# Kernel optimization log

Hardware: AMD Instinct MI355X
Metric: run time of the kernel (lower is better)

## Reference

```python
import jax, jax.numpy as jnp
import numpy as np
import math

B, T, C, D = 8, 2048, 1024, 1024
N_LAYER, LAYER_ID = 24, 12


def setup_inputs() -> dict:
    key = jax.random.key(0)
    ks = jax.random.split(key, 5)
    r01 = LAYER_ID / (N_LAYER - 1)
    r10 = 1.0 - LAYER_ID / N_LAYER
    ddd = np.arange(C, dtype=np.float64) / C                      # (C,)
    h = np.arange(D, dtype=np.float64)
    decay_speed = -5 + 8 * (h / (D - 1)) ** (0.7 + 1.3 * r01)     # time_decay init
    zigzag = ((np.arange(D) + 1) % 3 - 1) * 0.5
    time_first = np.log(0.3) + zigzag
    scale = C ** -0.5
    return {
        "x": jax.random.normal(ks[0], (B, T, C), jnp.float32),
        "time_decay": jnp.asarray(decay_speed, jnp.float32),
        "time_first": jnp.asarray(time_first, jnp.float32),
        "time_mix_k": jnp.asarray(ddd ** r10, jnp.float32),
        "time_mix_v": jnp.asarray(ddd ** r10 + 0.3 * r01, jnp.float32),
        "time_mix_r": jnp.asarray(ddd ** (0.5 * r10), jnp.float32),
        "Wk": jax.random.normal(ks[1], (D, C), jnp.float32) * scale,
        "Wv": jax.random.normal(ks[2], (D, C), jnp.float32) * scale,
        "Wr": jax.random.normal(ks[3], (D, C), jnp.float32) * scale,
        "Wo": jax.random.normal(ks[4], (C, D), jnp.float32) * scale,
    }


def _wkv(time_decay, time_first, k, v):
    # wkv_t = (e^{u+k_t} v_t + A_{t-1}) / (e^{u+k_t} + B_{t-1})
    # A_t = e^w A_{t-1} + e^{k_t} v_t ;  B_t likewise with v=1 ;  w = -exp(time_decay)
    # Exactly the math of the original conv1d-with-exp-curve trick, in O(T).
    ew = jnp.exp(-jnp.exp(time_decay))   # (D,)
    eu = jnp.exp(time_first)             # (D,)
    ek = jnp.exp(k)                      # [B,T,D]
    ekv = ek * v

    def step(carry, inp):
        a, b = carry                     # [B,D] each
        ekt, ekvt = inp                  # [B,D] each
        out = (eu * ekvt + a) / (eu * ekt + b)
        return (ew * a + ekvt, ew * b + ekt), out

    init = (jnp.zeros_like(ek[:, 0]), jnp.zeros_like(ek[:, 0]))
    xs = (jnp.swapaxes(ek, 0, 1), jnp.swapaxes(ekv, 0, 1))  # [T,B,D]
    _, out = jax.lax.scan(step, init, xs)
    return jnp.swapaxes(out, 0, 1)       # [B,T,D]


def reference(x, time_decay, time_first, time_mix_k, time_mix_v, time_mix_r, Wk, Wv, Wr, Wo):
    # time_shift: prepend zero row, drop last (ZeroPad2d((0,0,1,-1)))
    xx = jnp.pad(x, ((0, 0), (1, 0), (0, 0)))[:, :-1]
    xk = x * time_mix_k + xx * (1 - time_mix_k)
    xv = x * time_mix_v + xx * (1 - time_mix_v)
    xr = x * time_mix_r + xx * (1 - time_mix_r)
    k = jnp.einsum('btc,dc->btd', xk, Wk)
    v = jnp.einsum('btc,dc->btd', xv, Wv)
    sr = jax.nn.sigmoid(jnp.einsum('btc,dc->btd', xr, Wr))
    rwkv = sr * _wkv(time_decay, time_first, k, v)
    return jnp.einsum('btd,cd->btc', rwkv, Wo)
```

## Files before the change

kernel.cpp:

```cpp
#include <hip/hip_runtime.h>
#include <cstdint>
#include <cstddef>

#define Bb 8
#define Tt 2048
#define Cc 1024
#define Dd 1024
#define Mm (Bb*Tt)
#define CL 64
#define NCH (Tt/CL)


typedef __bf16  bf16x8  __attribute__((ext_vector_type(8)));
typedef float   floatx4 __attribute__((ext_vector_type(4)));

__device__ __forceinline__ ushort f2bf(float f) {
    unsigned u = __float_as_uint(f);
    u = (u + 0x7FFF + ((u >> 16) & 1)) >> 16;
    return (ushort)u;
}
__device__ __forceinline__ float bf2f(ushort u) {
    return __uint_as_float(((unsigned)u) << 16);
}

__device__ __forceinline__ void load_lds16(const void* g, void* l) {
    __builtin_amdgcn_global_load_lds((__attribute__((address_space(1))) void*)(g),
                                     (__attribute__((address_space(3))) void*)(l),
                                     16, 0, 0);
}

__global__ __launch_bounds__(256) void prep_mix3(
        const float* __restrict__ x,
        const float* __restrict__ mk, const float* __restrict__ mv,
        const float* __restrict__ mr,
        ushort* __restrict__ xk, ushort* __restrict__ xv, ushort* __restrict__ xr) {
    int i  = blockIdx.x * 256 + threadIdx.x;
    int cq = i & (Cc / 8 - 1);
    int m  = i >> 7;
    int t  = m & (Tt - 1);
    float xc[8], xp[8];
    *(float4*)&xc[0] = ((const float4*)x)[i * 2];
    *(float4*)&xc[4] = ((const float4*)x)[i * 2 + 1];
    if (t != 0) {
        *(float4*)&xp[0] = ((const float4*)x)[(i - Cc / 8) * 2];
        *(float4*)&xp[4] = ((const float4*)x)[(i - Cc / 8) * 2 + 1];
    } else {
#pragma unroll
        for (int j = 0; j < 8; j++) xp[j] = 0.f;
    }
    float wk[8], wv[8], wr[8];
    *(float4*)&wk[0] = ((const float4*)mk)[cq * 2];
    *(float4*)&wk[4] = ((const float4*)mk)[cq * 2 + 1];
    *(float4*)&wv[0] = ((const float4*)mv)[cq * 2];
    *(float4*)&wv[4] = ((const float4*)mv)[cq * 2 + 1];
    *(float4*)&wr[0] = ((const float4*)mr)[cq * 2];
    *(float4*)&wr[4] = ((const float4*)mr)[cq * 2 + 1];
    ushort ok[8], ov[8], orr[8];
#pragma unroll
    for (int j = 0; j < 8; j++) {
        float d = xc[j] - xp[j];
        ok[j]  = f2bf(xp[j] + d * wk[j]);
        ov[j]  = f2bf(xp[j] + d * wv[j]);
        orr[j] = f2bf(xp[j] + d * wr[j]);
    }
    ((ulonglong2*)xk)[i] = *(const ulonglong2*)ok;
    ((ulonglong2*)xv)[i] = *(const ulonglong2*)ov;
    ((ulonglong2*)xr)[i] = *(const ulonglong2*)orr;
}

__global__ __launch_bounds__(256) void cvt_w(
        const float* __restrict__ wk, const float* __restrict__ wv,
        const float* __restrict__ wr, const float* __restrict__ wo,
        ushort* __restrict__ ok, ushort* __restrict__ ov,
        ushort* __restrict__ orr, ushort* __restrict__ oo) {
    int i = blockIdx.x * 256 + threadIdx.x;
    int sel = i >> 18;
    int j = i & ((1 << 18) - 1);
    const float* s = sel == 0 ? wk : sel == 1 ? wv : sel == 2 ? wr : wo;
    ushort* d      = sel == 0 ? ok : sel == 1 ? ov : sel == 2 ? orr : oo;
    float4 f = ((const float4*)s)[j];
    ushort4 o;
    o.x = f2bf(f.x); o.y = f2bf(f.y); o.z = f2bf(f.z); o.w = f2bf(f.w);
    ((ushort4*)d)[j] = o;
}

struct GemmCore {
    floatx4 acc[4][4];
    int quad, fr, wave, wm, wn;

    __device__ __forceinline__ void run(
            const ushort* __restrict__ A, const ushort* __restrict__ Bw,
            long tm, long tn, int Kdim,
            __bf16* As, __bf16* Bs) {
        const int tid  = threadIdx.x;
        const int lane = tid & 63;
        quad = lane >> 4;
        fr   = lane & 15;
        wave = tid >> 6;
        wm   = (wave >> 1) * 64;
        wn   = (wave & 1) * 64;

        const int srow  = tid >> 2;
        const int spart = (tid & 3) ^ ((tid >> 3) & 3);
        const ushort* Ag0 = A + (tm + srow) * (long)Kdim + spart * 8;
        const ushort* Ag1 = Ag0 + 64 * (long)Kdim;
        const ushort* Bg0 = Bw + (tn + srow) * (long)Kdim + spart * 8;
        const ushort* Bg1 = Bg0 + 64 * (long)Kdim;
        const int swz = (fr >> 1) & 3;

        floatx4 zero = {0.f, 0.f, 0.f, 0.f};
#pragma unroll
        for (int a1 = 0; a1 < 4; a1++)
#pragma unroll
            for (int b1 = 0; b1 < 4; b1++) acc[a1][b1] = zero;

        const int niter = Kdim >> 5;
        load_lds16(Ag0, &As[wave * 512]);
        load_lds16(Ag1, &As[2048 + wave * 512]);
        load_lds16(Bg0, &Bs[wave * 512]);
        load_lds16(Bg1, &Bs[2048 + wave * 512]);

        for (int it = 0; it < niter; ++it) {
            const int cur = it & 1;
            __bf16* Ac = As + cur * 4096;
            __bf16* Bc = Bs + cur * 4096;
            __syncthreads();
            if (it + 1 < niter) {
                const int kt = (it + 1) << 5;
                __bf16* An = As + (cur ^ 1) * 4096;
                __bf16* Bn = Bs + (cur ^ 1) * 4096;
                load_lds16(Ag0 + kt, &An[wave * 512]);
                load_lds16(Ag1 + kt, &An[2048 + wave * 512]);
                load_lds16(Bg0 + kt, &Bn[wave * 512]);
                load_lds16(Bg1 + kt, &Bn[2048 + wave * 512]);
            }
            bf16x8 af[4], bfg[4];
#pragma unroll
            for (int mi = 0; mi < 4; mi++)
                af[mi] = *(const bf16x8*)&Ac[(wm + mi * 16 + fr) * 32 + (quad ^ swz) * 8];
#pragma unroll
            for (int ni = 0; ni < 4; ni++)
                bfg[ni] = *(const bf16x8*)&Bc[(wn + ni * 16 + fr) * 32 + (quad ^ swz) * 8];
#pragma unroll
            for (int mi = 0; mi < 4; mi++)
#pragma unroll
                for (int ni = 0; ni < 4; ni++)
                    acc[mi][ni] = __builtin_amdgcn_mfma_f32_16x16x32_bf16(
                        af[mi], bfg[ni], acc[mi][ni], 0, 0, 0);
        }
    }
};

template<int MODE>
__global__ __launch_bounds__(256) void gemm_nt(
        const ushort* __restrict__ A, const ushort* __restrict__ Bw,
        void* __restrict__ Co, int Ndim, int Kdim) {
    __shared__ __attribute__((aligned(16))) __bf16 As[2 * 128 * 32];
    __shared__ __attribute__((aligned(16))) __bf16 Bs[2 * 128 * 32];
    const long tm = (long)blockIdx.x * 128;
    const long tn = (long)blockIdx.y * 128;
    GemmCore g;
    g.run(A, Bw, tm, tn, Kdim, As, Bs);
#pragma unroll
    for (int mi = 0; mi < 4; mi++)
#pragma unroll
        for (int ni = 0; ni < 4; ni++)
#pragma unroll
            for (int r = 0; r < 4; r++) {
                long grow = tm + g.wm + mi * 16 + g.quad * 4 + r;
                long gcol = tn + g.wn + ni * 16 + g.fr;
                float v = g.acc[mi][ni][r];
                if (MODE == 2) v = 1.f / (1.f + __expf(-v));
                if (MODE == 0)      ((float*)Co)[grow * Ndim + gcol] = v;
                else if (MODE == 3) ((_Float16*)Co)[grow * Ndim + gcol] = (_Float16)v;
                else                ((ushort*)Co)[grow * Ndim + gcol] = f2bf(v);
            }
}

__global__ __launch_bounds__(256) void gemm3_nt(
        const ushort* __restrict__ xk, const ushort* __restrict__ xv,
        const ushort* __restrict__ xr,
        const ushort* __restrict__ wk, const ushort* __restrict__ wv,
        const ushort* __restrict__ wr,
        _Float16* __restrict__ kb, ushort* __restrict__ vb,
        ushort* __restrict__ sb) {
    __shared__ __attribute__((aligned(16))) __bf16 As[2 * 128 * 32];
    __shared__ __attribute__((aligned(16))) __bf16 Bs[2 * 128 * 32];
    const int proj = blockIdx.y >> 3;
    const long tm = (long)blockIdx.x * 128;
    const long tn = (long)(blockIdx.y & 7) * 128;
    const ushort* A  = proj == 0 ? xk : proj == 1 ? xv : xr;
    const ushort* Bw = proj == 0 ? wk : proj == 1 ? wv : wr;
    GemmCore g;
    g.run(A, Bw, tm, tn, Cc, As, Bs);
#pragma unroll
    for (int mi = 0; mi < 4; mi++)
#pragma unroll
        for (int ni = 0; ni < 4; ni++)
#pragma unroll
            for (int r = 0; r < 4; r++) {
                long grow = tm + g.wm + mi * 16 + g.quad * 4 + r;
                long gcol = tn + g.wn + ni * 16 + g.fr;
                long off = grow * Dd + gcol;
                float v = g.acc[mi][ni][r];
                if (proj == 0)      kb[off] = (_Float16)v;
                else if (proj == 1) vb[off] = f2bf(v);
                else                sb[off] = f2bf(1.f / (1.f + __expf(-v)));
            }
}

__global__ __launch_bounds__(256) void wkv_part(
        const _Float16* __restrict__ kb, const ushort* __restrict__ vb,
        const float* __restrict__ decay,
        float* __restrict__ pa, float* __restrict__ pb) {
    int gid = blockIdx.x * 256 + threadIdx.x;
    int d = gid & (Dd - 1);
    int c = (gid >> 10) & (NCH - 1);
    int b = gid >> 15;
    float ew = __expf(-__expf(decay[d]));
    size_t base = ((size_t)b * Tt + (size_t)c * CL) * Dd + d;
    float a = 0.f, bs = 0.f;
    for (int i0 = 0; i0 < CL; i0 += 8) {
        float kr[8], vr[8];
#pragma unroll
        for (int j = 0; j < 8; j++) {
            size_t idx = base + (size_t)(i0 + j) * Dd;
            kr[j] = (float)kb[idx]; vr[j] = bf2f(vb[idx]);
        }
#pragma unroll
        for (int j = 0; j < 8; j++) {
            float ek = __expf(kr[j]);
            a  = ew * a  + ek * vr[j];
            bs = ew * bs + ek;
        }
    }
    int sidx = c * (Bb * Dd) + b * Dd + d;
    pa[sidx] = a; pb[sidx] = bs;
}

__global__ __launch_bounds__(256) void wkv_prefix(
        const float* __restrict__ pa, const float* __restrict__ pb,
        const float* __restrict__ decay,
        float* __restrict__ sa, float* __restrict__ sb) {
    int gid = blockIdx.x * 256 + threadIdx.x;
    int d = gid & (Dd - 1);
    float ewL = __expf(-__expf(decay[d]) * (float)CL);
    float ca = 0.f, cb = 0.f;
#pragma unroll
    for (int c = 0; c < NCH; c++) {
        int idx = c * (Bb * Dd) + gid;
        sa[idx] = ca; sb[idx] = cb;
        ca = ewL * ca + pa[idx];
        cb = ewL * cb + pb[idx];
    }
}

__global__ __launch_bounds__(256) void wkv_chunk(
        const _Float16* __restrict__ kb, const ushort* __restrict__ vb,
        const ushort* __restrict__ sr,
        const float* __restrict__ decay, const float* __restrict__ tf,
        const float* __restrict__ sa, const float* __restrict__ sb,
        ushort* __restrict__ rw) {
    int gid = blockIdx.x * 256 + threadIdx.x;
    int d = gid & (Dd - 1);
    int c = (gid >> 10) & (NCH - 1);
    int b = gid >> 15;
    float ew = __expf(-__expf(decay[d]));
    float eu = __expf(tf[d]);
    int sidx = c * (Bb * Dd) + b * Dd + d;
    float a = sa[sidx], bs = sb[sidx];
    size_t base = ((size_t)b * Tt + (size_t)c * CL) * Dd + d;
    for (int i0 = 0; i0 < CL; i0 += 8) {
        float kr[8], vr[8], rr[8];
#pragma unroll
        for (int j = 0; j < 8; j++) {
            size_t idx = base + (size_t)(i0 + j) * Dd;
            kr[j] = (float)kb[idx]; vr[j] = bf2f(vb[idx]); rr[j] = bf2f(sr[idx]);
        }
#pragma unroll
        for (int j = 0; j < 8; j++) {
            float ek  = __expf(kr[j]);
            float ekv = ek * vr[j];
            float out = (eu * ekv + a) / (eu * ek + bs);
            a  = ew * a  + ekv;
            bs = ew * bs + ek;
            rw[base + (size_t)(i0 + j) * Dd] = f2bf(rr[j] * out);
        }
    }
}

extern "C" void kernel_launch(void* const* d_in, const int* in_sizes, int n_in,
                              void* d_out, int out_size, void* d_ws, size_t ws_size,
                              hipStream_t stream) {
    (void)in_sizes; (void)n_in; (void)out_size;
    const float* x  = (const float*)d_in[0];
    const float* td = (const float*)d_in[1];
    const float* tf = (const float*)d_in[2];
    const float* mk = (const float*)d_in[3];
    const float* mv = (const float*)d_in[4];
    const float* mr = (const float*)d_in[5];
    const float* Wk = (const float*)d_in[6];
    const float* Wv = (const float*)d_in[7];
    const float* Wr = (const float*)d_in[8];
    const float* Wo = (const float*)d_in[9];
    float* out = (float*)d_out;

    const size_t xsz = (size_t)Mm * Cc * 2;
    const size_t wsz = (size_t)Dd * Cc * 2;
    const size_t ssz = (size_t)Bb * NCH * Dd * 4;
    const size_t need_merged = 6 * xsz + 4 * wsz + 4 * ssz;

    char* p = (char*)d_ws;
    auto take = [&](size_t n) { char* r = p; p += n; return r; };
    ushort*   xk = (ushort*)take(xsz);
    ushort*   xv = (ushort*)take(xsz);
    ushort*   xr = (ushort*)take(xsz);
    _Float16* kb = (_Float16*)take(xsz);
    const bool merged = ws_size >= need_merged;
    ushort *vb, *sb, *rw;
    if (merged) {
        vb = (ushort*)take(xsz);
        sb = (ushort*)take(xsz);
        rw = xk;
    } else {
        vb = xk;
        sb = xv;
        rw = xr;
    }
    ushort* wk = (ushort*)take(wsz);
    ushort* wv = (ushort*)take(wsz);
    ushort* wr = (ushort*)take(wsz);
    ushort* wo = (ushort*)take(wsz);
    float*  pa = (float*)take(ssz);
    float*  pb = (float*)take(ssz);
    float*  sa = (float*)take(ssz);
    float*  sbst = (float*)take(ssz);

    dim3 g1(Mm / 128, Dd / 128);
    dim3 g2(Mm / 128, Cc / 128);
    dim3 g3(Mm / 128, 3 * Dd / 128);
    const int wkv_grid = (Bb * NCH * Dd) / 256;

    cvt_w<<<4096, 256, 0, stream>>>(Wk, Wv, Wr, Wo, wk, wv, wr, wo);
    prep_mix3<<<Mm * Cc / 8 / 256, 256, 0, stream>>>(x, mk, mv, mr, xk, xv, xr);

    if (merged) {
        gemm3_nt<<<g3, 256, 0, stream>>>(xk, xv, xr, wk, wv, wr, kb, vb, sb);
    } else {
        gemm_nt<3><<<g1, 256, 0, stream>>>(xk, wk, kb, Dd, Cc);
        gemm_nt<1><<<g1, 256, 0, stream>>>(xv, wv, vb, Dd, Cc);
        gemm_nt<2><<<g1, 256, 0, stream>>>(xr, wr, sb, Dd, Cc);
    }

    wkv_part  <<<wkv_grid, 256, 0, stream>>>(kb, vb, td, pa, pb);
    wkv_prefix<<<(Bb * Dd) / 256, 256, 0, stream>>>(pa, pb, td, sa, sbst);
    wkv_chunk <<<wkv_grid, 256, 0, stream>>>(kb, vb, sb, td, tf, sa, sbst, rw);

    gemm_nt<0><<<g2, 256, 0, stream>>>(rw, wo, out, Cc, Dd);
}
```

Before: 402.4 us.

## Enlarge GEMM tiles to 256x256 with 512 threads, triple-buffered LDS and XCD swizzle

The shared GEMM core grows from 128x128 tiles on 256 threads to 256x256 tiles on 512 threads (8 waves, each computing 128x64). The LDS pipeline goes from double to triple buffering with explicit vmcnt waits and raw barriers, and MFMA sections run at raised s_setprio. Block indices are remapped so that neighbouring tiles land on the same XCD. The goal is more operand reuse per byte loaded and better overlap of loads with compute. The cost is higher register pressure (32 accumulators per lane) and 96KB of LDS per block. The code also leaves redundant dead assignments to wm.

```diff
diff --git a/kernel.cpp b/kernel.cpp
--- a/kernel.cpp
+++ b/kernel.cpp
@@ -84,85 +84,124 @@
     ((ushort4*)d)[j] = o;
 }
 
-struct GemmCore {
-    floatx4 acc[4][4];
-    int quad, fr, wave, wm, wn;
+struct GemmCore256 {
+    floatx4 acc[8][4];
+    int quad, fr, wm, wn;
+
+    __device__ __forceinline__ void compute(const __bf16* __restrict__ Ac,
+                                            int goff) {
+        const __bf16* Bc = Ac + 8192;
+        bf16x8 af[8], bfr[4];
+#pragma unroll
+        for (int mi = 0; mi < 8; mi++)
+            af[mi] = *(const bf16x8*)&Ac[(wm + mi * 16 + fr) * 32 + goff];
+#pragma unroll
+        for (int ni = 0; ni < 4; ni++)
+            bfr[ni] = *(const bf16x8*)&Bc[(wn + ni * 16 + fr) * 32 + goff];
+        __builtin_amdgcn_s_setprio(1);
+#pragma unroll
+        for (int mi = 0; mi < 8; mi++)
+#pragma unroll
+            for (int ni = 0; ni < 4; ni++)
+                acc[mi][ni] = __builtin_amdgcn_mfma_f32_16x16x32_bf16(
+                    af[mi], bfr[ni], acc[mi][ni], 0, 0, 0);
+        __builtin_amdgcn_s_setprio(0);
+    }
 
     __device__ __forceinline__ void run(
             const ushort* __restrict__ A, const ushort* __restrict__ Bw,
-            long tm, long tn, int Kdim,
-            __bf16* As, __bf16* Bs) {
+            long tm, long tn, int Kdim, __bf16* LDSb) {
         const int tid  = threadIdx.x;
         const int lane = tid & 63;
         quad = lane >> 4;
         fr   = lane & 15;
-        wave = tid >> 6;
-        wm   = (wave >> 1) * 64;
-        wn   = (wave & 1) * 64;
+        const int wave = tid >> 6;
+        wm   = (wave >> 1) * 0;
+        wm   = (wave >> 1) * 0;
+        wm   = (wave & ~1) ? 0 : 0;
+        wm   = (wave >> 1) * 32;
+        wm   = ((wave >> 1)) * 32;
+        wm   = (wave >> 1) * 32;
+        {
+            const int wave_m = wave >> 1;
+            (void)wave_m;
+        }
+        wm = (wave >> 2) * 128;
+        wn = (wave & 3) * 64;
+        const int swz  = (fr >> 1) & 3;
+        const int goff = (quad ^ swz) * 8;
 
         const int srow  = tid >> 2;
         const int spart = (tid & 3) ^ ((tid >> 3) & 3);
         const ushort* Ag0 = A + (tm + srow) * (long)Kdim + spart * 8;
-        const ushort* Ag1 = Ag0 + 64 * (long)Kdim;
+        const ushort* Ag1 = Ag0 + 128 * (long)Kdim;
         const ushort* Bg0 = Bw + (tn + srow) * (long)Kdim + spart * 8;
-        const ushort* Bg1 = Bg0 + 64 * (long)Kdim;
-        const int swz = (fr >> 1) & 3;
+        const ushort* Bg1 = Bg0 + 128 * (long)Kdim;
+        const int wlds = wave * 512;
 
         floatx4 zero = {0.f, 0.f, 0.f, 0.f};
 #pragma unroll
-        for (int a1 = 0; a1 < 4; a1++)
+        for (int a1 = 0; a1 < 8; a1++)
 #pragma unroll
             for (int b1 = 0; b1 < 4; b1++) acc[a1][b1] = zero;
 
-        const int niter = Kdim >> 5;
-        load_lds16(Ag0, &As[wave * 512]);
-        load_lds16(Ag1, &As[2048 + wave * 512]);
-        load_lds16(Bg0, &Bs[wave * 512]);
-        load_lds16(Bg1, &Bs[2048 + wave * 512]);
-
-        for (int it = 0; it < niter; ++it) {
-            const int cur = it & 1;
-            __bf16* Ac = As + cur * 4096;
-            __bf16* Bc = Bs + cur * 4096;
-            __syncthreads();
-            if (it + 1 < niter) {
-                const int kt = (it + 1) << 5;
-                __bf16* An = As + (cur ^ 1) * 4096;
-                __bf16* Bn = Bs + (cur ^ 1) * 4096;
-                load_lds16(Ag0 + kt, &An[wave * 512]);
-                load_lds16(Ag1 + kt, &An[2048 + wave * 512]);
-                load_lds16(Bg0 + kt, &Bn[wave * 512]);
-                load_lds16(Bg1 + kt, &Bn[2048 + wave * 512]);
+        const int NT = Kdim >> 5;
+
+        {
+            __bf16* b0 = LDSb;
+            load_lds16(Ag0,      b0 + wlds);
+            load_lds16(Ag1,      b0 + 4096  + wlds);
+            load_lds16(Bg0,      b0 + 8192  + wlds);
+            load_lds16(Bg1,      b0 + 12288 + wlds);
+            __bf16* b1 = LDSb + 16384;
+            load_lds16(Ag0 + 32, b1 + wlds);
+            load_lds16(Ag1 + 32, b1 + 4096  + wlds);
+            load_lds16(Bg0 + 32, b1 + 8192  + wlds);
+            load_lds16(Bg1 + 32, b1 + 12288 + wlds);
+        }
+
+        int bcur = 0, bst = 2;
+        for (int T = 0; T < NT - 1; ++T) {
+            asm volatile("s_waitcnt vmcnt(4) lgkmcnt(0)" ::: "memory");
+            __builtin_amdgcn_s_barrier();
+            asm volatile("" ::: "memory");
+            if (T < NT - 2) {
+                const int kt = (T + 2) << 5;
+                __bf16* nb = LDSb + bst * 16384;
+                load_lds16(Ag0 + kt, nb + wlds);
+                load_lds16(Ag1 + kt, nb + 4096  + wlds);
+                load_lds16(Bg0 + kt, nb + 8192  + wlds);
+                load_lds16(Bg1 + kt, nb + 12288 + wlds);
             }
-            bf16x8 af[4], bfg[4];
-#pragma unroll
-            for (int mi = 0; mi < 4; mi++)
-                af[mi] = *(const bf16x8*)&Ac[(wm + mi * 16 + fr) * 32 + (quad ^ swz) * 8];
-#pragma unroll
-            for (int ni = 0; ni < 4; ni++)
-                bfg[ni] = *(const bf16x8*)&Bc[(wn + ni * 16 + fr) * 32 + (quad ^ swz) * 8];
-#pragma unroll
-            for (int mi = 0; mi < 4; mi++)
-#pragma unroll
-                for (int ni = 0; ni < 4; ni++)
-                    acc[mi][ni] = __builtin_amdgcn_mfma_f32_16x16x32_bf16(
-                        af[mi], bfg[ni], acc[mi][ni], 0, 0, 0);
-        }
+            compute(LDSb + bcur * 16384, goff);
+            if (++bcur == 3) bcur = 0;
+            if (++bst == 3) bst = 0;
+        }
+        asm volatile("s_waitcnt vmcnt(0) lgkmcnt(0)" ::: "memory");
+        __builtin_amdgcn_s_barrier();
+        asm volatile("" ::: "memory");
+        compute(LDSb + bcur * 16384, goff);
     }
 };
 
+__device__ __forceinline__ int xcd_swizzle(int nwg) {
+    const int orig  = blockIdx.y * 64 + blockIdx.x;
+    const int chunk = nwg >> 3;
+    return (orig & 7) * chunk + (orig >> 3);
+}
+
 template<int MODE>
-__global__ __launch_bounds__(256) void gemm_nt(
+__global__ __launch_bounds__(512, 2) void gemm_nt(
         const ushort* __restrict__ A, const ushort* __restrict__ Bw,
         void* __restrict__ Co, int Ndim, int Kdim) {
-    __shared__ __attribute__((aligned(16))) __bf16 As[2 * 128 * 32];
-    __shared__ __attribute__((aligned(16))) __bf16 Bs[2 * 128 * 32];
-    const long tm = (long)blockIdx.x * 128;
-    const long tn = (long)blockIdx.y * 128;
-    GemmCore g;
-    g.run(A, Bw, tm, tn, Kdim, As, Bs);
-#pragma unroll
-    for (int mi = 0; mi < 4; mi++)
+    __shared__ __attribute__((aligned(16))) __bf16 LDSb[3 * 16384];
+    const int swz = xcd_swizzle(gridDim.x * gridDim.y);
+    const long tm = (long)(swz & 63) * 256;
+    const long tn = (long)(swz >> 6) * 256;
+    GemmCore256 g;
+    g.run(A, Bw, tm, tn, Kdim, LDSb);
+#pragma unroll
+    for (int mi = 0; mi < 8; mi++)
 #pragma unroll
         for (int ni = 0; ni < 4; ni++)
 #pragma unroll
@@ -177,24 +216,26 @@
             }
 }
 
-__global__ __launch_bounds__(256) void gemm3_nt(
+__global__ __launch_bounds__(512, 2) void gemm3_nt(
         const ushort* __restrict__ xk, const ushort* __restrict__ xv,
         const ushort* __restrict__ xr,
         const ushort* __restrict__ wk, const ushort* __restrict__ wv,
         const ushort* __restrict__ wr,
         _Float16* __restrict__ kb, ushort* __restrict__ vb,
         ushort* __restrict__ sb) {
-    __shared__ __attribute__((aligned(16))) __bf16 As[2 * 128 * 32];
-    __shared__ __attribute__((aligned(16))) __bf16 Bs[2 * 128 * 32];
-    const int proj = blockIdx.y >> 3;
-    const long tm = (long)blockIdx.x * 128;
-    const long tn = (long)(blockIdx.y & 7) * 128;
+    __shared__ __attribute__((aligned(16))) __bf16 LDSb[3 * 16384];
+    const int swz = xcd_swizzle(64 * 12);
+    const int mt  = swz & 63;
+    const int yt  = swz >> 6;
+    const int proj = yt >> 2;
+    const long tm = (long)mt * 256;
+    const long tn = (long)(yt & 3) * 256;
     const ushort* A  = proj == 0 ? xk : proj == 1 ? xv : xr;
     const ushort* Bw = proj == 0 ? wk : proj == 1 ? wv : wr;
-    GemmCore g;
-    g.run(A, Bw, tm, tn, Cc, As, Bs);
-#pragma unroll
-    for (int mi = 0; mi < 4; mi++)
+    GemmCore256 g;
+    g.run(A, Bw, tm, tn, Cc, LDSb);
+#pragma unroll
+    for (int mi = 0; mi < 8; mi++)
 #pragma unroll
         for (int ni = 0; ni < 4; ni++)
 #pragma unroll
@@ -336,25 +377,25 @@
     float*  sa = (float*)take(ssz);
     float*  sbst = (float*)take(ssz);
 
-    dim3 g1(Mm / 128, Dd / 128);
-    dim3 g2(Mm / 128, Cc / 128);
-    dim3 g3(Mm / 128, 3 * Dd / 128);
+    dim3 g1(Mm / 256, Dd / 256);
+    dim3 g2(Mm / 256, Cc / 256);
+    dim3 g3(Mm / 256, 3 * Dd / 256);
     const int wkv_grid = (Bb * NCH * Dd) / 256;
 
     cvt_w<<<4096, 256, 0, stream>>>(Wk, Wv, Wr, Wo, wk, wv, wr, wo);
     prep_mix3<<<Mm * Cc / 8 / 256, 256, 0, stream>>>(x, mk, mv, mr, xk, xv, xr);
 
     if (merged) {
-        gemm3_nt<<<g3, 256, 0, stream>>>(xk, xv, xr, wk, wv, wr, kb, vb, sb);
+        gemm3_nt<<<g3, 512, 0, stream>>>(xk, xv, xr, wk, wv, wr, kb, vb, sb);
     } else {
-        gemm_nt<3><<<g1, 256, 0, stream>>>(xk, wk, kb, Dd, Cc);
-        gemm_nt<1><<<g1, 256, 0, stream>>>(xv, wv, vb, Dd, Cc);
-        gemm_nt<2><<<g1, 256, 0, stream>>>(xr, wr, sb, Dd, Cc);
+        gemm_nt<3><<<g1, 512, 0, stream>>>(xk, wk, kb, Dd, Cc);
+        gemm_nt<1><<<g1, 512, 0, stream>>>(xv, wv, vb, Dd, Cc);
+        gemm_nt<2><<<g1, 512, 0, stream>>>(xr, wr, sb, Dd, Cc);
     }
 
     wkv_part  <<<wkv_grid, 256, 0, stream>>>(kb, vb, td, pa, pb);
     wkv_prefix<<<(Bb * Dd) / 256, 256, 0, stream>>>(pa, pb, td, sa, sbst);
     wkv_chunk <<<wkv_grid, 256, 0, stream>>>(kb, vb, sb, td, tf, sa, sbst, rw);
 
-    gemm_nt<0><<<g2, 256, 0, stream>>>(rw, wo, out, Cc, Dd);
-}
+    gemm_nt<0><<<g2, 512, 0, stream>>>(rw, wo, out, Cc, Dd);
+}
```

Result: faster. 386.9 us (-3.8%).
